# Kernel optimization log

Measured on AMD Instinct MI355X. Metric: run time of the kernel, lower is better.

Reference implementation:

```python
import jax, jax.numpy as jnp
import numpy as np
import math

N, E, R = 50000, 800000, 32
DIN = 128
H, D = 8, 16          # num_heads, head_dim; H*D == out_ent_feats == 128
HOP = 5
ALPHA = 0.1
EPS = 1e-5


def layer_norm(x, g, b):
    m = jnp.mean(x, axis=-1, keepdims=True)
    v = jnp.mean((x - m) ** 2, axis=-1, keepdims=True)
    return (x - m) * jax.lax.rsqrt(v + EPS) * g + b


def segment_softmax(e, dst, num_nodes):
    # e: [E, H] scores, softmax over incoming edges of each dst node
    m = jax.ops.segment_max(e, dst, num_segments=num_nodes)      # [N, H]
    ex = jnp.exp(e - m[dst])
    s = jax.ops.segment_sum(ex, dst, num_segments=num_nodes)     # [N, H]
    return ex / s[dst]


def setup_inputs() -> dict:
    key = jax.random.key(0)
    ks = jax.random.split(key, 12)
    gain = 0.02  # small init scale (small_init_gain-style)
    ent_feat = jax.random.normal(ks[0], (N, DIN), dtype=jnp.float32)
    rel_feat = jax.random.normal(ks[1], (R, DIN), dtype=jnp.float32)
    src = jax.random.randint(ks[2], (E,), 0, N, dtype=jnp.int32)
    # guarantee every node has in-degree >= 1 (DGL raises otherwise)
    dst_rand = jax.random.randint(ks[3], (E - N,), 0, N, dtype=jnp.int32)
    dst = jnp.concatenate([jnp.arange(N, dtype=jnp.int32), dst_rand])
    rid = jax.random.randint(ks[4], (E,), 0, R, dtype=jnp.int32)
    W_head = jax.random.normal(ks[5], (DIN, H * D), dtype=jnp.float32) * gain
    W_tail = jax.random.normal(ks[6], (DIN, H * D), dtype=jnp.float32) * gain
    W_ent = jax.random.normal(ks[7], (DIN, H * D), dtype=jnp.float32) * gain
    W_rel = jax.random.normal(ks[8], (DIN, H * D), dtype=jnp.float32) * gain
    attn_r = jax.random.normal(ks[9], (1, H, D), dtype=jnp.float32) * gain
    W1 = jax.random.normal(ks[10], (H * D, 4 * H * D), dtype=jnp.float32) * gain
    W2 = jax.random.normal(ks[11], (4 * H * D, H * D), dtype=jnp.float32) * gain
    return dict(
        ent_feat=ent_feat, rel_feat=rel_feat, src=src, dst=dst, rid=rid,
        W_head=W_head, W_tail=W_tail, W_ent=W_ent, W_rel=W_rel, attn_r=attn_r,
        ln_ent_g=jnp.ones((DIN,), jnp.float32), ln_ent_b=jnp.zeros((DIN,), jnp.float32),
        ln_rel_g=jnp.ones((DIN,), jnp.float32), ln_rel_b=jnp.zeros((DIN,), jnp.float32),
        ff_ln_g=jnp.ones((H * D,), jnp.float32), ff_ln_b=jnp.zeros((H * D,), jnp.float32),
        W1=W1, b1=jnp.zeros((4 * H * D,), jnp.float32),
        W2=W2, b2=jnp.zeros((H * D,), jnp.float32),
    )


def _forward(ent_feat, rel_feat, src, dst, rid,
             W_head, W_tail, W_ent, W_rel, attn_r,
             ln_ent_g, ln_ent_b, ln_rel_g, ln_rel_b, ff_ln_g, ff_ln_b,
             W1, b1, W2, b2):
    n = ent_feat.shape[0]
    x = layer_norm(ent_feat, ln_ent_g, ln_ent_b)
    feat_head = (x @ W_head).reshape(n, H, D)
    feat_tail = (x @ W_tail).reshape(n, H, D)
    feat_ent = (x @ W_ent).reshape(n, H, D)

    # per-edge dot-product attention score: u_dot_v('eh','et')
    e = jnp.sum(feat_head[src] * feat_tail[dst], axis=-1)          # [E, H]

    r = layer_norm(rel_feat, ln_rel_g, ln_rel_b)
    feat_rel = (r @ W_rel).reshape(R, H, D)
    er = jnp.sum(feat_rel * attn_r, axis=-1)                       # [R, H]
    e = e * er[rid]                                                # [E, H]

    # e_mul_v with log_in = log(in_degree) of dst node
    deg = jax.ops.segment_sum(jnp.ones((e.shape[0],), e.dtype), dst, num_segments=n)
    log_in = jnp.log(jnp.maximum(deg, 1.0))                        # [N]
    e = e * log_in[dst][:, None] / math.sqrt(D)

    a = segment_softmax(e, dst, n)                                 # [E, H]

    # PPR diffusion: feat <- (1-alpha) * A^T feat + alpha * feat_0
    feat = feat_ent
    for _ in range(HOP):
        msg = feat[src] * a[:, :, None]                            # [E, H, D]
        agg = jax.ops.segment_sum(msg, dst, num_segments=n)        # [N, H, D]
        feat = (1.0 - ALPHA) * agg + ALPHA * feat_ent

    # residual (Identity: in_ent_feats == out_ent_feats)
    rst = feat + ent_feat.reshape(n, H, D)
    rst = rst.reshape(n, H * D)

    h = layer_norm(rst, ff_ln_g, ff_ln_b)
    ff = jax.nn.relu(h @ W1 + b1) @ W2 + b2
    return ff + rst


def reference(ent_feat, rel_feat, src, dst, rid,
              W_head, W_tail, W_ent, W_rel, attn_r,
              ln_ent_g, ln_ent_b, ln_rel_g, ln_rel_b, ff_ln_g, ff_ln_b,
              W1, b1, W2, b2):
    return _forward(ent_feat, rel_feat, src, dst, rid,
                    W_head, W_tail, W_ent, W_rel, attn_r,
                    ln_ent_g, ln_ent_b, ln_rel_g, ln_rel_b, ff_ln_g, ff_ln_b,
                    W1, b1, W2, b2)
```

## Files before the change

### kernel.cpp

```cpp
#include <hip/hip_runtime.h>
#include <hip/hip_bf16.h>

#define N_NODES 50000
#define N_EDGES 800000
#define N_REL 32
#define DIN 128
#define NH 8
#define HD 16
#define FF_HID 512
#define EPS_LN 1e-5f

typedef __attribute__((ext_vector_type(8))) short bf16x8;
typedef __attribute__((ext_vector_type(4))) float f32x4;
typedef __attribute__((ext_vector_type(2))) float f32x2;
typedef unsigned short ushort_t;
typedef unsigned int uint_t;

static __device__ __forceinline__ unsigned short f2bf(float f) {
    union { float f; unsigned u; } v; v.f = f;
    unsigned r = (v.u + 0x7fffu + ((v.u >> 16) & 1u)) >> 16;
    return (unsigned short)r;
}
static __device__ __forceinline__ float bf2f(unsigned u16) {
    union { unsigned u; float f; } v; v.u = u16 << 16; return v.f;
}
static __device__ __forceinline__ unsigned char f2fp8(float f) {
    return (unsigned char)(__builtin_amdgcn_cvt_pk_fp8_f32(f, f, 0, false) & 0xff);
}
static __device__ __forceinline__ ushort_t f2fp8x2(float x0, float x1) {
    return (ushort_t)(__builtin_amdgcn_cvt_pk_fp8_f32(x0, x1, 0, false) & 0xffff);
}

static __device__ __forceinline__ void pack_dev(const float* __restrict__ W,
                                                short* __restrict__ out, int K, int Ncols,
                                                int idx) {
    int KT = K >> 5;
    int l = idx & 63;
    int tile = idx >> 6;
    int kt = tile & (KT - 1);
    int ct = tile / KT;
    int c = ct * 16 + (l & 15);
    int k0 = kt * 32 + ((l >> 4) * 8);
    bf16x8 v;
#pragma unroll
    for (int j = 0; j < 8; j++) v[j] = (short)f2bf(W[(size_t)(k0 + j) * Ncols + c]);
    *(bf16x8*)(out + (size_t)idx * 8) = v;
}

#define C0_HIST 512
__global__ __launch_bounds__(256) void combo0_kernel(
    const int* __restrict__ dst, int* __restrict__ deg, const float* __restrict__ W1,
    short* __restrict__ W1p, const float* __restrict__ W2, short* __restrict__ W2p,
    const float* __restrict__ Wh, short* __restrict__ Whp, const float* __restrict__ Wt,
    short* __restrict__ Wtp, const float* __restrict__ We, short* __restrict__ Wep,
    const float* __restrict__ rel_feat, const float* __restrict__ gr,
    const float* __restrict__ br, const float* __restrict__ W_rel,
    const float* __restrict__ attn_r, float* __restrict__ er) {
    __shared__ float red[128];
    __shared__ float xsr[128];
    __shared__ float prod[128];
    int b = blockIdx.x, tid = threadIdx.x;
    if (b < C0_HIST) {
        int i = b * 256 + tid;
        int stride = C0_HIST * 256;
        for (; i < N_EDGES; i += stride) atomicAdd(&deg[dst[i]], 1);
    } else if (b < C0_HIST + 32) {
        pack_dev(W1, W1p, DIN, FF_HID, (b - C0_HIST) * 256 + tid);
    } else if (b < C0_HIST + 64) {
        pack_dev(W2, W2p, FF_HID, DIN, (b - C0_HIST - 32) * 256 + tid);
    } else if (b < C0_HIST + 72) {
        pack_dev(Wh, Whp, DIN, DIN, (b - C0_HIST - 64) * 256 + tid);
    } else if (b < C0_HIST + 80) {
        pack_dev(Wt, Wtp, DIN, DIN, (b - C0_HIST - 72) * 256 + tid);
    } else if (b < C0_HIST + 88) {
        pack_dev(We, Wep, DIN, DIN, (b - C0_HIST - 80) * 256 + tid);
    } else {
        int r = b - (C0_HIST + 88);
        float x = 0.f;
        if (tid < 128) {
            x = rel_feat[r * DIN + tid];
            red[tid] = x;
        }
        __syncthreads();
        for (int off = 64; off > 0; off >>= 1) {
            if (tid < off) red[tid] += red[tid + off];
            __syncthreads();
        }
        float mean = red[0] * (1.f / DIN);
        __syncthreads();
        if (tid < 128) red[tid] = x * x;
        __syncthreads();
        for (int off = 64; off > 0; off >>= 1) {
            if (tid < off) red[tid] += red[tid + off];
            __syncthreads();
        }
        float var = red[0] * (1.f / DIN) - mean * mean;
        float rs = rsqrtf(var + EPS_LN);
        if (tid < 128) xsr[tid] = (x - mean) * rs * gr[tid] + br[tid];
        __syncthreads();
        if (tid < 128) {
            float acc = 0.f;
            for (int k = 0; k < DIN; k++) acc += xsr[k] * W_rel[k * DIN + tid];
            prod[tid] = acc * attn_r[tid];
        }
        __syncthreads();
        if (tid < NH) {
            float s = 0.f;
            for (int d = 0; d < HD; d++) s += prod[tid * HD + d];
            er[r * NH + tid] = s;
        }
    }
}

__global__ __launch_bounds__(1024) void scan2_kernel(const int* __restrict__ deg,
                                                     int* __restrict__ row_off, int n) {
    __shared__ int lds[1024];
    __shared__ int wsum[16];
    __shared__ int s_base;
    int b = blockIdx.x, tid = threadIdx.x;
    int start = b * 1024;
    int partial = 0;
    for (int i = tid; i < start; i += 1024) partial += deg[i];
    for (int m = 32; m > 0; m >>= 1) partial += __shfl_down(partial, m);
    int wid = tid >> 6, lane = tid & 63;
    if (lane == 0) wsum[wid] = partial;
    __syncthreads();
    if (tid == 0) {
        int s = 0;
#pragma unroll
        for (int w = 0; w < 16; w++) s += wsum[w];
        s_base = s;
    }
    int i = start + tid;
    int v = (i < n) ? deg[i] : 0;
    lds[tid] = v;
    __syncthreads();
    for (int off = 1; off < 1024; off <<= 1) {
        int t = (tid >= off) ? lds[tid - off] : 0;
        __syncthreads();
        lds[tid] += t;
        __syncthreads();
    }
    int base = s_base;
    if (i < n) row_off[i] = base + lds[tid] - v;
    if (i == n - 1) row_off[n] = base + lds[tid];
}

#define C1_SCAT 1024
__global__ __launch_bounds__(256) void combo1_kernel(
    const int* __restrict__ src, const int* __restrict__ dst, const int* __restrict__ rid,
    const int* __restrict__ row_off, int* __restrict__ cursor, int* __restrict__ sr_perm,
    const float* __restrict__ ent, const float* __restrict__ g, const float* __restrict__ b,
    const short* __restrict__ Whp, const short* __restrict__ Wtp,
    const short* __restrict__ Wep, unsigned char* __restrict__ head_fp8,
    ushort_t* __restrict__ tail_bf, ushort_t* __restrict__ entp_bf,
    unsigned char* __restrict__ entp_fp8) {
    __shared__ float xs[32][128];
    __shared__ short hsb[32][136];
    int blk = blockIdx.x, tid = threadIdx.x;
    if (blk < C1_SCAT) {
        int i = blk * 256 + tid;
        int stride = C1_SCAT * 256;
        for (; i < N_EDGES; i += stride) {
            int u = dst[i];
            int p = row_off[u] + atomicAdd(&cursor[u], 1);
            sr_perm[p] = src[i] | (rid[i] << 16);
        }
        return;
    }
    int base = (blk - C1_SCAT) * 32;
    {
        int c = tid & 127, rb = tid >> 7;
#pragma unroll
        for (int j = 0; j < 16; j++) {
            int r = j * 2 + rb;
            int row = base + r;
            xs[r][c] = (row < N_NODES) ? ent[(size_t)row * DIN + c] : 0.f;
        }
    }
    __syncthreads();
    int wave = tid >> 6, lane = tid & 63;
    {
        float g0 = g[lane], g1 = g[lane + 64], bb0 = b[lane], bb1 = b[lane + 64];
        for (int r = wave * 8; r < wave * 8 + 8; r++) {
            float x0 = xs[r][lane], x1 = xs[r][lane + 64];
            float s1 = x0 + x1, s2 = x0 * x0 + x1 * x1;
            for (int m = 1; m < 64; m <<= 1) {
                s1 += __shfl_xor(s1, m);
                s2 += __shfl_xor(s2, m);
            }
            float mean = s1 * (1.f / DIN);
            float var = s2 * (1.f / DIN) - mean * mean;
            float rs = rsqrtf(var + EPS_LN);
            hsb[r][lane] = (short)f2bf((x0 - mean) * rs * g0 + bb0);
            hsb[r][lane + 64] = (short)f2bf((x1 - mean) * rs * g1 + bb1);
        }
    }
    __syncthreads();
    bf16x8 a[2][4];
#pragma unroll
    for (int rt = 0; rt < 2; rt++)
#pragma unroll
        for (int kt = 0; kt < 4; kt++)
            a[rt][kt] = *(const bf16x8*)&hsb[rt * 16 + (lane & 15)][kt * 32 + (lane >> 4) * 8];
#pragma unroll
    for (int m = 0; m < 3; m++) {
        const bf16x8* bp = (m == 0)   ? (const bf16x8*)Whp
                           : (m == 1) ? (const bf16x8*)Wtp
                                      : (const bf16x8*)Wep;
#pragma unroll
        for (int c2 = 0; c2 < 2; c2++) {
            int ct = wave * 2 + c2;
            f32x4 acc0 = {0.f, 0.f, 0.f, 0.f}, acc1 = {0.f, 0.f, 0.f, 0.f};
#pragma unroll
            for (int kt = 0; kt < 4; kt++) {
                bf16x8 bf = bp[(ct * 4 + kt) * 64 + lane];
                acc0 = __builtin_amdgcn_mfma_f32_16x16x32_bf16(a[0][kt], bf, acc0, 0, 0, 0);
                acc1 = __builtin_amdgcn_mfma_f32_16x16x32_bf16(a[1][kt], bf, acc1, 0, 0, 0);
            }
            int col = ct * 16 + (lane & 15);
            int r0 = (lane >> 4) * 4;
#pragma unroll
            for (int j = 0; j < 4; j++) {
                int row0 = base + r0 + j, row1 = base + 16 + r0 + j;
                if (m == 0) {
                    if (row0 < N_NODES) head_fp8[(size_t)row0 * DIN + col] = f2fp8(acc0[j]);
                    if (row1 < N_NODES) head_fp8[(size_t)row1 * DIN + col] = f2fp8(acc1[j]);
                } else if (m == 1) {
                    if (row0 < N_NODES) tail_bf[(size_t)row0 * DIN + col] = f2bf(acc0[j]);
                    if (row1 < N_NODES) tail_bf[(size_t)row1 * DIN + col] = f2bf(acc1[j]);
                } else {
                    if (row0 < N_NODES) {
                        entp_bf[(size_t)row0 * DIN + col] = f2bf(acc0[j]);
                        entp_fp8[(size_t)row0 * DIN + col] = f2fp8(acc0[j]);
                    }
                    if (row1 < N_NODES) {
                        entp_bf[(size_t)row1 * DIN + col] = f2bf(acc1[j]);
                        entp_fp8[(size_t)row1 * DIN + col] = f2fp8(acc1[j]);
                    }
                }
            }
        }
    }
}

__global__ __launch_bounds__(256) void scores_kernel(
    const unsigned char* __restrict__ head_fp8, const ushort_t* __restrict__ tail_bf,
    const float* __restrict__ er, const int* __restrict__ row_off,
    const int* __restrict__ sr_perm, ushort_t* __restrict__ a_bf,
    float* __restrict__ inv9) {
    int wid = threadIdx.x >> 6;
    int u = blockIdx.x * 4 + wid;
    int lane = threadIdx.x & 63;
    int h = lane & 7, esub = lane >> 3;
    int p0 = row_off[u], p1 = row_off[u + 1];
    int deg = p1 - p0;
    float scale = logf((float)(deg > 0 ? deg : 1)) * 0.25f;
    float t[16];
    {
        const uint_t* tp = (const uint_t*)(tail_bf + (size_t)u * DIN + h * HD);
#pragma unroll
        for (int i = 0; i < 8; i++) {
            uint_t w = tp[i];
            t[2 * i] = bf2f(w & 0xffffu);
            t[2 * i + 1] = bf2f(w >> 16);
        }
    }
    float ssum = 0.f;
    for (int p = p0 + esub; p < p1; p += 8) {
        int v = sr_perm[p];
        int s = v & 0xffff;
        int rr = v >> 16;
        const uint_t* hp = (const uint_t*)(head_fp8 + (size_t)s * DIN + h * HD);
        float dot = 0.f;
#pragma unroll
        for (int i = 0; i < 4; i++) {
            uint_t w = hp[i];
            f32x2 lo = __builtin_amdgcn_cvt_pk_f32_fp8(w, false);
            f32x2 hi = __builtin_amdgcn_cvt_pk_f32_fp8(w, true);
            dot += lo.x * t[4 * i] + lo.y * t[4 * i + 1] + hi.x * t[4 * i + 2] +
                   hi.y * t[4 * i + 3];
        }
        float e = dot * er[rr * NH + h] * scale;
        float sx = expf(e);
        a_bf[(size_t)p * NH + h] = f2bf(sx);
        ssum += sx;
    }
    ssum += __shfl_xor(ssum, 8);
    ssum += __shfl_xor(ssum, 16);
    ssum += __shfl_xor(ssum, 32);
    if (lane < 8) inv9[(size_t)u * NH + lane] = 0.9f / ssum;
}

template <bool OUT_BF>
__global__ __launch_bounds__(256) void diffuse8_kernel(
    const unsigned char* __restrict__ fin8, const ushort_t* __restrict__ entp_bf,
    const ushort_t* __restrict__ a_bf, const int* __restrict__ sr_perm,
    const int* __restrict__ row_off, const float* __restrict__ inv9,
    void* __restrict__ fout) {
    int wid = threadIdx.x >> 6;
    int u = blockIdx.x * 4 + wid;
    int lane = threadIdx.x & 63;
    int hh = lane >> 3;
    int p0 = row_off[u], p1 = row_off[u + 1];
    float acc0 = 0.f, acc1 = 0.f;
    int p = p0;
    for (; p + 4 <= p1; p += 4) {
        int s0 = sr_perm[p] & 0xffff, s1 = sr_perm[p + 1] & 0xffff;
        int s2 = sr_perm[p + 2] & 0xffff, s3 = sr_perm[p + 3] & 0xffff;
        float a0 = bf2f(a_bf[(size_t)p * NH + hh]);
        float a1 = bf2f(a_bf[(size_t)(p + 1) * NH + hh]);
        float a2 = bf2f(a_bf[(size_t)(p + 2) * NH + hh]);
        float a3 = bf2f(a_bf[(size_t)(p + 3) * NH + hh]);
        uint_t w0 = *(const ushort_t*)(fin8 + (size_t)s0 * DIN + 2 * lane);
        uint_t w1 = *(const ushort_t*)(fin8 + (size_t)s1 * DIN + 2 * lane);
        uint_t w2 = *(const ushort_t*)(fin8 + (size_t)s2 * DIN + 2 * lane);
        uint_t w3 = *(const ushort_t*)(fin8 + (size_t)s3 * DIN + 2 * lane);
        f32x2 v0 = __builtin_amdgcn_cvt_pk_f32_fp8(w0, false);
        f32x2 v1 = __builtin_amdgcn_cvt_pk_f32_fp8(w1, false);
        f32x2 v2 = __builtin_amdgcn_cvt_pk_f32_fp8(w2, false);
        f32x2 v3 = __builtin_amdgcn_cvt_pk_f32_fp8(w3, false);
        acc0 += a0 * v0.x + a1 * v1.x + a2 * v2.x + a3 * v3.x;
        acc1 += a0 * v0.y + a1 * v1.y + a2 * v2.y + a3 * v3.y;
    }
    for (; p < p1; ++p) {
        int s0 = sr_perm[p] & 0xffff;
        float a0 = bf2f(a_bf[(size_t)p * NH + hh]);
        uint_t w0 = *(const ushort_t*)(fin8 + (size_t)s0 * DIN + 2 * lane);
        f32x2 v0 = __builtin_amdgcn_cvt_pk_f32_fp8(w0, false);
        acc0 += a0 * v0.x;
        acc1 += a0 * v0.y;
    }
    float iv = inv9[(size_t)u * NH + hh];
    size_t o = (size_t)u * DIN + 2 * lane;
    uint_t e = *(const uint_t*)(entp_bf + o);
    float x0 = iv * acc0 + 0.1f * bf2f(e & 0xffffu);
    float x1 = iv * acc1 + 0.1f * bf2f(e >> 16);
    if (OUT_BF) {
        *(uint_t*)((ushort_t*)fout + o) = (uint_t)f2bf(x0) | ((uint_t)f2bf(x1) << 16);
    } else {
        *(ushort_t*)((unsigned char*)fout + o) = f2fp8x2(x0, x1);
    }
}

static __device__ __forceinline__ int hid_idx(int row, int col) {
    return row * 512 + ((((col >> 3) & 63) ^ (row & 7)) << 3) + (col & 7);
}
__global__ __launch_bounds__(256) void ffn_mfma_kernel(
    const ushort_t* __restrict__ feat, const float* __restrict__ ent0,
    const float* __restrict__ g, const float* __restrict__ b,
    const short* __restrict__ W1p, const float* __restrict__ b1,
    const short* __restrict__ W2p, const float* __restrict__ b2,
    float* __restrict__ out) {
    __shared__ ushort_t rst_bf[32][136];
    __shared__ short hs[32][136];
    __shared__ short hid[32 * 512];
    int tid = threadIdx.x;
    int base = blockIdx.x * 32;
    int wave = tid >> 6, lane = tid & 63;
    {
        int c = tid & 127, rb = tid >> 7;
#pragma unroll
        for (int j = 0; j < 16; j++) {
            int r = j * 2 + rb;
            int row = base + r;
            float v = 0.f;
            if (row < N_NODES) {
                size_t idx = (size_t)row * DIN + c;
                v = bf2f(feat[idx]) + ent0[idx];
            }
            rst_bf[r][c] = f2bf(v);
        }
    }
    __syncthreads();
    {
        float g0 = g[lane], g1 = g[lane + 64], bb0 = b[lane], bb1 = b[lane + 64];
        for (int r = wave * 8; r < wave * 8 + 8; r++) {
            float x0 = bf2f(rst_bf[r][lane]), x1 = bf2f(rst_bf[r][lane + 64]);
            float s1 = x0 + x1, s2 = x0 * x0 + x1 * x1;
            for (int m = 1; m < 64; m <<= 1) {
                s1 += __shfl_xor(s1, m);
                s2 += __shfl_xor(s2, m);
            }
            float mean = s1 * (1.f / DIN);
            float var = s2 * (1.f / DIN) - mean * mean;
            float rs = rsqrtf(var + EPS_LN);
            hs[r][lane] = (short)f2bf((x0 - mean) * rs * g0 + bb0);
            hs[r][lane + 64] = (short)f2bf((x1 - mean) * rs * g1 + bb1);
        }
    }
    __syncthreads();
    {
        bf16x8 a[2][4];
#pragma unroll
        for (int rt = 0; rt < 2; rt++)
#pragma unroll
            for (int kt = 0; kt < 4; kt++)
                a[rt][kt] =
                    *(const bf16x8*)&hs[rt * 16 + (lane & 15)][kt * 32 + (lane >> 4) * 8];
        const bf16x8* bp = (const bf16x8*)W1p;
        for (int cti = 0; cti < 8; cti++) {
            int ct = wave * 8 + cti;
            f32x4 acc0 = {0.f, 0.f, 0.f, 0.f}, acc1 = {0.f, 0.f, 0.f, 0.f};
#pragma unroll
            for (int kt = 0; kt < 4; kt++) {
                bf16x8 bf = bp[(ct * 4 + kt) * 64 + lane];
                acc0 = __builtin_amdgcn_mfma_f32_16x16x32_bf16(a[0][kt], bf, acc0, 0, 0, 0);
                acc1 = __builtin_amdgcn_mfma_f32_16x16x32_bf16(a[1][kt], bf, acc1, 0, 0, 0);
            }
            int col = ct * 16 + (lane & 15);
            float bv = b1[col];
            int r0 = (lane >> 4) * 4;
#pragma unroll
            for (int j = 0; j < 4; j++) {
                hid[hid_idx(r0 + j, col)] = (short)f2bf(fmaxf(acc0[j] + bv, 0.f));
                hid[hid_idx(16 + r0 + j, col)] = (short)f2bf(fmaxf(acc1[j] + bv, 0.f));
            }
        }
    }
    __syncthreads();
    {
        f32x4 acc[2][2] = {{{0.f, 0.f, 0.f, 0.f}, {0.f, 0.f, 0.f, 0.f}},
                           {{0.f, 0.f, 0.f, 0.f}, {0.f, 0.f, 0.f, 0.f}}};
        const bf16x8* bp2 = (const bf16x8*)W2p;
        for (int kt = 0; kt < 16; kt++) {
            int row0 = lane & 15, row1 = 16 + (lane & 15);
            int col8 = kt * 32 + (lane >> 4) * 8;
            bf16x8 a0 = *(const bf16x8*)&hid[hid_idx(row0, col8)];
            bf16x8 a1 = *(const bf16x8*)&hid[hid_idx(row1, col8)];
#pragma unroll
            for (int c2 = 0; c2 < 2; c2++) {
                int ct = wave * 2 + c2;
                bf16x8 bf = bp2[(ct * 16 + kt) * 64 + lane];
                acc[0][c2] = __builtin_amdgcn_mfma_f32_16x16x32_bf16(a0, bf, acc[0][c2], 0, 0, 0);
                acc[1][c2] = __builtin_amdgcn_mfma_f32_16x16x32_bf16(a1, bf, acc[1][c2], 0, 0, 0);
            }
        }
#pragma unroll
        for (int rt = 0; rt < 2; rt++)
#pragma unroll
            for (int c2 = 0; c2 < 2; c2++) {
                int col = (wave * 2 + c2) * 16 + (lane & 15);
                float bv = b2[col];
                int r0 = rt * 16 + (lane >> 4) * 4;
#pragma unroll
                for (int j = 0; j < 4; j++) {
                    int row = base + r0 + j;
                    if (row < N_NODES)
                        out[(size_t)row * DIN + col] =
                            acc[rt][c2][j] + bv + bf2f(rst_bf[r0 + j][col]);
                }
            }
    }
}

extern "C" void kernel_launch(void* const* d_in, const int* in_sizes, int n_in,
                              void* d_out, int out_size, void* d_ws, size_t ws_size,
                              hipStream_t stream) {
    const float* ent_feat = (const float*)d_in[0];
    const float* rel_feat = (const float*)d_in[1];
    const int* src = (const int*)d_in[2];
    const int* dst = (const int*)d_in[3];
    const int* rid = (const int*)d_in[4];
    const float* W_head = (const float*)d_in[5];
    const float* W_tail = (const float*)d_in[6];
    const float* W_ent = (const float*)d_in[7];
    const float* W_rel = (const float*)d_in[8];
    const float* attn_r = (const float*)d_in[9];
    const float* ln_ent_g = (const float*)d_in[10];
    const float* ln_ent_b = (const float*)d_in[11];
    const float* ln_rel_g = (const float*)d_in[12];
    const float* ln_rel_b = (const float*)d_in[13];
    const float* ff_ln_g = (const float*)d_in[14];
    const float* ff_ln_b = (const float*)d_in[15];
    const float* W1 = (const float*)d_in[16];
    const float* b1 = (const float*)d_in[17];
    const float* W2 = (const float*)d_in[18];
    const float* b2 = (const float*)d_in[19];
    float* out = (float*)d_out;

    const int N = N_NODES, E = N_EDGES;

    char* cur = (char*)d_ws;
    auto alloc = [&](size_t bytes, size_t align) -> void* {
        uintptr_t p = (uintptr_t)cur;
        p = (p + align - 1) & ~(uintptr_t)(align - 1);
        cur = (char*)(p + bytes);
        return (void*)p;
    };
    ushort_t* tail_bf = (ushort_t*)alloc((size_t)N * DIN * 2, 16);
    ushort_t* entp_bf = (ushort_t*)alloc((size_t)N * DIN * 2, 16);
    unsigned char* entp_fp8 = (unsigned char*)alloc((size_t)N * DIN, 16);
    unsigned char* f8A = (unsigned char*)alloc((size_t)N * DIN, 16);
    unsigned char* f8B = (unsigned char*)alloc((size_t)N * DIN, 16);
    unsigned char* head_fp8 = (unsigned char*)alloc((size_t)N * DIN, 16);
    int* sr_perm = (int*)alloc((size_t)E * 4, 16);
    int* row_off = (int*)alloc((size_t)(N + 1) * 4, 16);
    int* deg = (int*)alloc((size_t)2 * N * 4, 16);
    int* cursor = deg + N;
    float* er = (float*)alloc((size_t)N_REL * NH * 4, 16);
    float* inv9 = (float*)alloc((size_t)N * NH * 4, 16);
    short* W1p = (short*)alloc((size_t)DIN * FF_HID * 2, 16);
    short* W2p = (short*)alloc((size_t)FF_HID * DIN * 2, 16);
    short* Whp = (short*)alloc((size_t)DIN * DIN * 2, 16);
    short* Wtp = (short*)alloc((size_t)DIN * DIN * 2, 16);
    short* Wep = (short*)alloc((size_t)DIN * DIN * 2, 16);
    ushort_t* a_fit = (ushort_t*)alloc((size_t)E * NH * 2, 16);
    ushort_t* a_bf = ((size_t)(cur - (char*)d_ws) <= ws_size) ? a_fit : (ushort_t*)d_out;

    hipMemsetAsync(deg, 0, sizeof(int) * 2 * (size_t)N, stream);
    combo0_kernel<<<632, 256, 0, stream>>>(dst, deg, W1, W1p, W2, W2p, W_head, Whp,
                                           W_tail, Wtp, W_ent, Wep, rel_feat, ln_rel_g,
                                           ln_rel_b, W_rel, attn_r, er);
    scan2_kernel<<<(N + 1023) / 1024, 1024, 0, stream>>>(deg, row_off, N);
    int nblk32 = (N + 31) / 32;
    combo1_kernel<<<C1_SCAT + nblk32, 256, 0, stream>>>(
        src, dst, rid, row_off, cursor, sr_perm, ent_feat, ln_ent_g, ln_ent_b, Whp, Wtp,
        Wep, head_fp8, tail_bf, entp_bf, entp_fp8);
    scores_kernel<<<N / 4, 256, 0, stream>>>(head_fp8, tail_bf, er, row_off, sr_perm,
                                             a_bf, inv9);
    diffuse8_kernel<false><<<N / 4, 256, 0, stream>>>(entp_fp8, entp_bf, a_bf, sr_perm,
                                                      row_off, inv9, f8A);
    diffuse8_kernel<false><<<N / 4, 256, 0, stream>>>(f8A, entp_bf, a_bf, sr_perm,
                                                      row_off, inv9, f8B);
    diffuse8_kernel<false><<<N / 4, 256, 0, stream>>>(f8B, entp_bf, a_bf, sr_perm,
                                                      row_off, inv9, f8A);
    diffuse8_kernel<false><<<N / 4, 256, 0, stream>>>(f8A, entp_bf, a_bf, sr_perm,
                                                      row_off, inv9, f8B);
    diffuse8_kernel<true><<<N / 4, 256, 0, stream>>>(f8B, entp_bf, a_bf, sr_perm,
                                                     row_off, inv9, tail_bf);
    ffn_mfma_kernel<<<nblk32, 256, 0, stream>>>(tail_bf, ent_feat, ff_ln_g, ff_ln_b, W1p,
                                                b1, W2p, b2, out);
}
```

Measured before the change: 367.9 us.

## Partition edge scatter by dst range, unroll diffusion 8x, halve FFN tile rows

The CSR scatter now runs 8192 blocks. Each block scans one slice of edges and handles only those whose destination falls in one of 8 node ranges, so concurrent atomics and writes stay local to that range. The cost is reading each edge 8 times. The diffusion inner loop is unrolled to 8 edges so more gather loads are in flight at once. The FFN kernel uses 16-row tiles instead of 32, which lowers LDS use and doubles the block count for occupancy but halves weight reuse per block.

```diff
diff --git a/kernel.cpp b/kernel.cpp
--- a/kernel.cpp
+++ b/kernel.cpp
@@ -146,7 +146,8 @@
     if (i == n - 1) row_off[n] = base + lds[tid];
 }
 
-#define C1_SCAT 1024
+#define C1_SCAT 8192
+#define NRANGE_DIV 6250
 __global__ __launch_bounds__(256) void combo1_kernel(
     const int* __restrict__ src, const int* __restrict__ dst, const int* __restrict__ rid,
     const int* __restrict__ row_off, int* __restrict__ cursor, int* __restrict__ sr_perm,
@@ -159,12 +160,18 @@
     __shared__ short hsb[32][136];
     int blk = blockIdx.x, tid = threadIdx.x;
     if (blk < C1_SCAT) {
-        int i = blk * 256 + tid;
-        int stride = C1_SCAT * 256;
-        for (; i < N_EDGES; i += stride) {
+        const int chunk = (N_EDGES + 1023) / 1024;
+        int range = blk & 7;
+        int slice = blk >> 3;
+        int lo = range * NRANGE_DIV, hi = lo + NRANGE_DIV;
+        int i0 = slice * chunk;
+        int i1 = min(i0 + chunk, N_EDGES);
+        for (int i = i0 + tid; i < i1; i += 256) {
             int u = dst[i];
-            int p = row_off[u] + atomicAdd(&cursor[u], 1);
-            sr_perm[p] = src[i] | (rid[i] << 16);
+            if (u >= lo && u < hi) {
+                int p = row_off[u] + atomicAdd(&cursor[u], 1);
+                sr_perm[p] = src[i] | (rid[i] << 16);
+            }
         }
         return;
     }
@@ -305,23 +312,23 @@
     int p0 = row_off[u], p1 = row_off[u + 1];
     float acc0 = 0.f, acc1 = 0.f;
     int p = p0;
-    for (; p + 4 <= p1; p += 4) {
-        int s0 = sr_perm[p] & 0xffff, s1 = sr_perm[p + 1] & 0xffff;
-        int s2 = sr_perm[p + 2] & 0xffff, s3 = sr_perm[p + 3] & 0xffff;
-        float a0 = bf2f(a_bf[(size_t)p * NH + hh]);
-        float a1 = bf2f(a_bf[(size_t)(p + 1) * NH + hh]);
-        float a2 = bf2f(a_bf[(size_t)(p + 2) * NH + hh]);
-        float a3 = bf2f(a_bf[(size_t)(p + 3) * NH + hh]);
-        uint_t w0 = *(const ushort_t*)(fin8 + (size_t)s0 * DIN + 2 * lane);
-        uint_t w1 = *(const ushort_t*)(fin8 + (size_t)s1 * DIN + 2 * lane);
-        uint_t w2 = *(const ushort_t*)(fin8 + (size_t)s2 * DIN + 2 * lane);
-        uint_t w3 = *(const ushort_t*)(fin8 + (size_t)s3 * DIN + 2 * lane);
-        f32x2 v0 = __builtin_amdgcn_cvt_pk_f32_fp8(w0, false);
-        f32x2 v1 = __builtin_amdgcn_cvt_pk_f32_fp8(w1, false);
-        f32x2 v2 = __builtin_amdgcn_cvt_pk_f32_fp8(w2, false);
-        f32x2 v3 = __builtin_amdgcn_cvt_pk_f32_fp8(w3, false);
-        acc0 += a0 * v0.x + a1 * v1.x + a2 * v2.x + a3 * v3.x;
-        acc1 += a0 * v0.y + a1 * v1.y + a2 * v2.y + a3 * v3.y;
+    for (; p + 8 <= p1; p += 8) {
+        int sv[8];
+        float av[8];
+        ushort_t wv[8];
+#pragma unroll
+        for (int k = 0; k < 8; k++) sv[k] = sr_perm[p + k] & 0xffff;
+#pragma unroll
+        for (int k = 0; k < 8; k++) av[k] = bf2f(a_bf[(size_t)(p + k) * NH + hh]);
+#pragma unroll
+        for (int k = 0; k < 8; k++)
+            wv[k] = *(const ushort_t*)(fin8 + (size_t)sv[k] * DIN + 2 * lane);
+#pragma unroll
+        for (int k = 0; k < 8; k++) {
+            f32x2 v = __builtin_amdgcn_cvt_pk_f32_fp8(wv[k], false);
+            acc0 += av[k] * v.x;
+            acc1 += av[k] * v.y;
+        }
     }
     for (; p < p1; ++p) {
         int s0 = sr_perm[p] & 0xffff;
@@ -352,16 +359,16 @@
     const short* __restrict__ W1p, const float* __restrict__ b1,
     const short* __restrict__ W2p, const float* __restrict__ b2,
     float* __restrict__ out) {
-    __shared__ ushort_t rst_bf[32][136];
-    __shared__ short hs[32][136];
-    __shared__ short hid[32 * 512];
+    __shared__ ushort_t rst_bf[16][136];
+    __shared__ short hs[16][136];
+    __shared__ short hid[16 * 512];
     int tid = threadIdx.x;
-    int base = blockIdx.x * 32;
+    int base = blockIdx.x * 16;
     int wave = tid >> 6, lane = tid & 63;
     {
         int c = tid & 127, rb = tid >> 7;
 #pragma unroll
-        for (int j = 0; j < 16; j++) {
+        for (int j = 0; j < 8; j++) {
             int r = j * 2 + rb;
             int row = base + r;
             float v = 0.f;
@@ -375,7 +382,7 @@
     __syncthreads();
     {
         float g0 = g[lane], g1 = g[lane + 64], bb0 = b[lane], bb1 = b[lane + 64];
-        for (int r = wave * 8; r < wave * 8 + 8; r++) {
+        for (int r = wave * 4; r < wave * 4 + 4; r++) {
             float x0 = bf2f(rst_bf[r][lane]), x1 = bf2f(rst_bf[r][lane + 64]);
             float s1 = x0 + x1, s2 = x0 * x0 + x1 * x1;
             for (int m = 1; m < 64; m <<= 1) {
@@ -391,66 +398,53 @@
     }
     __syncthreads();
     {
-        bf16x8 a[2][4];
-#pragma unroll
-        for (int rt = 0; rt < 2; rt++)
-#pragma unroll
-            for (int kt = 0; kt < 4; kt++)
-                a[rt][kt] =
-                    *(const bf16x8*)&hs[rt * 16 + (lane & 15)][kt * 32 + (lane >> 4) * 8];
+        bf16x8 a[4];
+#pragma unroll
+        for (int kt = 0; kt < 4; kt++)
+            a[kt] = *(const bf16x8*)&hs[lane & 15][kt * 32 + (lane >> 4) * 8];
         const bf16x8* bp = (const bf16x8*)W1p;
         for (int cti = 0; cti < 8; cti++) {
             int ct = wave * 8 + cti;
-            f32x4 acc0 = {0.f, 0.f, 0.f, 0.f}, acc1 = {0.f, 0.f, 0.f, 0.f};
+            f32x4 acc0 = {0.f, 0.f, 0.f, 0.f};
 #pragma unroll
             for (int kt = 0; kt < 4; kt++) {
                 bf16x8 bf = bp[(ct * 4 + kt) * 64 + lane];
-                acc0 = __builtin_amdgcn_mfma_f32_16x16x32_bf16(a[0][kt], bf, acc0, 0, 0, 0);
-                acc1 = __builtin_amdgcn_mfma_f32_16x16x32_bf16(a[1][kt], bf, acc1, 0, 0, 0);
+                acc0 = __builtin_amdgcn_mfma_f32_16x16x32_bf16(a[kt], bf, acc0, 0, 0, 0);
             }
             int col = ct * 16 + (lane & 15);
             float bv = b1[col];
             int r0 = (lane >> 4) * 4;
 #pragma unroll
-            for (int j = 0; j < 4; j++) {
+            for (int j = 0; j < 4; j++)
                 hid[hid_idx(r0 + j, col)] = (short)f2bf(fmaxf(acc0[j] + bv, 0.f));
-                hid[hid_idx(16 + r0 + j, col)] = (short)f2bf(fmaxf(acc1[j] + bv, 0.f));
-            }
-        }
-    }
-    __syncthreads();
-    {
-        f32x4 acc[2][2] = {{{0.f, 0.f, 0.f, 0.f}, {0.f, 0.f, 0.f, 0.f}},
-                           {{0.f, 0.f, 0.f, 0.f}, {0.f, 0.f, 0.f, 0.f}}};
+        }
+    }
+    __syncthreads();
+    {
+        f32x4 acc[2] = {{0.f, 0.f, 0.f, 0.f}, {0.f, 0.f, 0.f, 0.f}};
         const bf16x8* bp2 = (const bf16x8*)W2p;
         for (int kt = 0; kt < 16; kt++) {
-            int row0 = lane & 15, row1 = 16 + (lane & 15);
             int col8 = kt * 32 + (lane >> 4) * 8;
-            bf16x8 a0 = *(const bf16x8*)&hid[hid_idx(row0, col8)];
-            bf16x8 a1 = *(const bf16x8*)&hid[hid_idx(row1, col8)];
+            bf16x8 a0 = *(const bf16x8*)&hid[hid_idx(lane & 15, col8)];
 #pragma unroll
             for (int c2 = 0; c2 < 2; c2++) {
                 int ct = wave * 2 + c2;
                 bf16x8 bf = bp2[(ct * 16 + kt) * 64 + lane];
-                acc[0][c2] = __builtin_amdgcn_mfma_f32_16x16x32_bf16(a0, bf, acc[0][c2], 0, 0, 0);
-                acc[1][c2] = __builtin_amdgcn_mfma_f32_16x16x32_bf16(a1, bf, acc[1][c2], 0, 0, 0);
-            }
-        }
-#pragma unroll
-        for (int rt = 0; rt < 2; rt++)
-#pragma unroll
-            for (int c2 = 0; c2 < 2; c2++) {
-                int col = (wave * 2 + c2) * 16 + (lane & 15);
-                float bv = b2[col];
-                int r0 = rt * 16 + (lane >> 4) * 4;
-#pragma unroll
-                for (int j = 0; j < 4; j++) {
-                    int row = base + r0 + j;
-                    if (row < N_NODES)
-                        out[(size_t)row * DIN + col] =
-                            acc[rt][c2][j] + bv + bf2f(rst_bf[r0 + j][col]);
-                }
-            }
+                acc[c2] = __builtin_amdgcn_mfma_f32_16x16x32_bf16(a0, bf, acc[c2], 0, 0, 0);
+            }
+        }
+#pragma unroll
+        for (int c2 = 0; c2 < 2; c2++) {
+            int col = (wave * 2 + c2) * 16 + (lane & 15);
+            float bv = b2[col];
+            int r0 = (lane >> 4) * 4;
+#pragma unroll
+            for (int j = 0; j < 4; j++) {
+                int row = base + r0 + j;
+                if (row < N_NODES)
+                    out[(size_t)row * DIN + col] = acc[c2][j] + bv + bf2f(rst_bf[r0 + j][col]);
+            }
+        }
     }
 }
 
@@ -529,6 +523,7 @@
                                                       row_off, inv9, f8B);
     diffuse8_kernel<true><<<N / 4, 256, 0, stream>>>(f8B, entp_bf, a_bf, sr_perm,
                                                      row_off, inv9, tail_bf);
-    ffn_mfma_kernel<<<nblk32, 256, 0, stream>>>(tail_bf, ent_feat, ff_ln_g, ff_ln_b, W1p,
+    int nblk16 = (N + 15) / 16;
+    ffn_mfma_kernel<<<nblk16, 256, 0, stream>>>(tail_bf, ent_feat, ff_ln_g, ff_ln_b, W1p,
                                                 b1, W2p, b2, out);
 }
```

Result: no change. 365.5 us (-0.7%).
